# Kernel optimization log

Measured on AMD Instinct MI355X. Metric: run time of the kernel, lower is better.

The kernel has to match this reference:

```python
import jax, jax.numpy as jnp
from jax import lax
import numpy as np

B, T, D_IN, H = 4096, 512, 1, 16


def _lstm_layer(x_seq, W_ih, W_hh, b_ih, b_hh):
    """One LSTM layer, batch_first. x_seq: [B,T,D] -> [B,T,H].
    PyTorch gate order: i, f, g, o. Zero initial (h, c)."""
    H_ = W_hh.shape[1]
    # Precompute input contribution for all timesteps (one big GEMM).
    pre = jnp.einsum('btd,gd->btg', x_seq, W_ih) + b_ih + b_hh  # [B,T,4H]

    def step(carry, p_t):
        h, c = carry
        gates = p_t + h @ W_hh.T  # [B,4H]
        i, f, g, o = jnp.split(gates, 4, axis=-1)
        i = jax.nn.sigmoid(i)
        f = jax.nn.sigmoid(f)
        g = jnp.tanh(g)
        o = jax.nn.sigmoid(o)
        c = f * c + i * g
        h = o * jnp.tanh(c)
        return (h, c), h

    b = x_seq.shape[0]
    init = (jnp.zeros((b, H_), x_seq.dtype), jnp.zeros((b, H_), x_seq.dtype))
    _, hs = lax.scan(step, init, jnp.swapaxes(pre, 0, 1))  # hs: [T,B,H]
    return jnp.swapaxes(hs, 0, 1)


def setup_inputs() -> dict:
    key = jax.random.key(0)
    ks = jax.random.split(key, 11)
    s_ih0 = 1.0 / np.sqrt(H)
    inp = {
        'x': jax.random.normal(ks[0], (B, T, D_IN), dtype=jnp.float32),
        # layer 0: input_dim -> H
        'W_ih0': jax.random.uniform(ks[1], (4 * H, D_IN), jnp.float32, -s_ih0, s_ih0),
        'W_hh0': jax.random.uniform(ks[2], (4 * H, H), jnp.float32, -s_ih0, s_ih0),
        'b_ih0': jax.random.uniform(ks[3], (4 * H,), jnp.float32, -s_ih0, s_ih0),
        'b_hh0': jax.random.uniform(ks[4], (4 * H,), jnp.float32, -s_ih0, s_ih0),
        # layer 1: H -> H
        'W_ih1': jax.random.uniform(ks[5], (4 * H, H), jnp.float32, -s_ih0, s_ih0),
        'W_hh1': jax.random.uniform(ks[6], (4 * H, H), jnp.float32, -s_ih0, s_ih0),
        'b_ih1': jax.random.uniform(ks[7], (4 * H,), jnp.float32, -s_ih0, s_ih0),
        'b_hh1': jax.random.uniform(ks[8], (4 * H,), jnp.float32, -s_ih0, s_ih0),
        # fc head: H -> 1
        'W_fc': jax.random.uniform(ks[9], (1, H), jnp.float32, -s_ih0, s_ih0),
        'b_fc': jax.random.uniform(ks[10], (1,), jnp.float32, -s_ih0, s_ih0),
    }
    return inp


def reference(x, W_ih0, W_hh0, b_ih0, b_hh0, W_ih1, W_hh1, b_ih1, b_hh1, W_fc, b_fc):
    h0 = _lstm_layer(x, W_ih0, W_hh0, b_ih0, b_hh0)   # [B,T,H]
    h1 = _lstm_layer(h0, W_ih1, W_hh1, b_ih1, b_hh1)  # [B,T,H]
    last = h1[:, -1, :]                               # [B,H]
    return last @ W_fc.T + b_fc                       # [B,1]
```

## Files before the change

### kernel.cpp

```cpp
#include <hip/hip_runtime.h>
#include <math.h>

#define TT 512
#define LOG2E 1.4426950408889634f

__device__ __forceinline__ float fast_rcp(float v)  { return __builtin_amdgcn_rcpf(v); }
__device__ __forceinline__ float fast_exp2(float v) { return __builtin_amdgcn_exp2f(v); }

__global__ __launch_bounds__(64, 2)
void lstm2_wave(const float* __restrict__ x,
                const float* __restrict__ W_ih0, const float* __restrict__ W_hh0,
                const float* __restrict__ b_ih0, const float* __restrict__ b_hh0,
                const float* __restrict__ W_ih1, const float* __restrict__ W_hh1,
                const float* __restrict__ b_ih1, const float* __restrict__ b_hh1,
                const float* __restrict__ W_fc,  const float* __restrict__ b_fc,
                float* __restrict__ out)
{
    const int l    = threadIdx.x;
    const int grp  = l >> 5;
    const int half = (l >> 4) & 1;
    const int j    = l & 15;
    const int bid  = blockIdx.x;

    const int ra0 = half * 16 + j;
    const int ra1 = ra0 + 32;

    __shared__ float lds[1168];

    {
        const float4* xg = (const float4*)(x + (size_t)bid * 1024);
        float4* xl = (float4*)&lds[144];
        xl[l]       = xg[l];
        xl[l + 64]  = xg[l + 64];
        xl[l + 128] = xg[l + 128];
        xl[l + 192] = xg[l + 192];
    }
    __syncthreads();

    const float bb0a = b_ih0[ra0] + b_hh0[ra0];
    const float bb0b = b_ih0[ra1] + b_hh0[ra1];
    const float bb1a = b_ih1[ra0] + b_hh1[ra0];
    const float bb1b = b_ih1[ra1] + b_hh1[ra1];
    const float wxa  = W_ih0[ra0];
    const float wxb  = W_ih0[ra1];
    const float Ca1 = half ? (-LOG2E) : (-2.0f * LOG2E);
    const float Aa1 = half ? 1.0f : 2.0f;
    const float Ba1 = half ? 0.0f : -1.0f;
    const float nl2e = -LOG2E;

    const int widx = half ? (80 + grp * 32 + j) : (grp * 40 + j);

    float cs0, cs1 = 0.0f;
    {
        const float x0 = lds[144 + grp * 512];
        const float a_s0 = fmaf(x0, wxa, bb0a);
        const float a_s1 = fmaf(x0, wxb, bb0b);
        const float s0 = fast_rcp(1.0f + fast_exp2(a_s0 * nl2e));
        const float s1 = fmaf(Aa1, fast_rcp(1.0f + fast_exp2(a_s1 * Ca1)), Ba1);
        const float p0 = s0 * s1;
        cs0 = p0;
        const float e = fast_exp2(fabsf(cs0) * (2.0f * LOG2E));
        float th = fmaf(-2.0f, fast_rcp(e + 1.0f), 1.0f);
        th = copysignf(th, cs0);
        const float osw = __shfl_xor(s1, 16);
        const float h0v = osw * th;
        lds[widx]      = h0v;
        lds[widx + 16] = 0.0f;
    }

    {
        unsigned base = (unsigned)(size_t)(void*)&lds[0];
        unsigned hb   = base + grp * 160;
        unsigned xa   = base + 576 + grp * 2048 + 4;
        unsigned wb_  = base + widx * 4;
        const float* pwa = W_hh0 + ra0 * 16;
        const float* pwb = W_ih1 + ra0 * 16;
        const float* pwc = W_hh1 + ra0 * 16;

        asm volatile(
            "s_waitcnt lgkmcnt(0)\n"
            "global_load_dwordx4 v[80:83],   %[pwa], off\n"
            "global_load_dwordx4 v[84:87],   %[pwa], off offset:16\n"
            "global_load_dwordx4 v[88:91],   %[pwa], off offset:32\n"
            "global_load_dwordx4 v[92:95],   %[pwa], off offset:48\n"
            "global_load_dwordx4 v[96:99],   %[pwa], off offset:2048\n"
            "global_load_dwordx4 v[100:103], %[pwa], off offset:2064\n"
            "global_load_dwordx4 v[104:107], %[pwa], off offset:2080\n"
            "global_load_dwordx4 v[108:111], %[pwa], off offset:2096\n"
            "global_load_dwordx4 v[112:115], %[pwb], off\n"
            "global_load_dwordx4 v[116:119], %[pwb], off offset:16\n"
            "global_load_dwordx4 v[120:123], %[pwb], off offset:32\n"
            "global_load_dwordx4 v[124:127], %[pwb], off offset:48\n"
            "global_load_dwordx4 v[128:131], %[pwb], off offset:2048\n"
            "global_load_dwordx4 v[132:135], %[pwb], off offset:2064\n"
            "global_load_dwordx4 v[136:139], %[pwb], off offset:2080\n"
            "global_load_dwordx4 v[140:143], %[pwb], off offset:2096\n"
            "global_load_dwordx4 v[144:147], %[pwc], off\n"
            "global_load_dwordx4 v[148:151], %[pwc], off offset:16\n"
            "global_load_dwordx4 v[152:155], %[pwc], off offset:32\n"
            "global_load_dwordx4 v[156:159], %[pwc], off offset:48\n"
            "global_load_dwordx4 v[160:163], %[pwc], off offset:2048\n"
            "global_load_dwordx4 v[164:167], %[pwc], off offset:2064\n"
            "global_load_dwordx4 v[168:171], %[pwc], off offset:2080\n"
            "global_load_dwordx4 v[172:175], %[pwc], off offset:2096\n"
            "v_mov_b32 v24, %[wb]\n"
            "v_mov_b32 v25, %[hb]\n"
            "v_mov_b32 v26, %[xa]\n"
            "v_mov_b32 v176, %[c0i]\n"
            "v_mov_b32 v177, %[c1]\n"
            "s_movk_i32 s22, 511\n"
            "s_mov_b32 s20, 0x7fffffff\n"
            "s_mov_b32 s21, 0x4038aa3b\n"
            "s_waitcnt vmcnt(0)\n"
            "Llstm_%=:\n"
            "ds_read_b128 v[32:35], v25\n"
            "ds_read_b128 v[36:39], v25 offset:16\n"
            "ds_read_b128 v[40:43], v25 offset:32\n"
            "ds_read_b128 v[44:47], v25 offset:48\n"
            "ds_read_b128 v[48:51], v25 offset:64\n"
            "ds_read_b128 v[52:55], v25 offset:80\n"
            "ds_read_b128 v[56:59], v25 offset:96\n"
            "ds_read_b128 v[60:63], v25 offset:112\n"
            "ds_read_b32  v27, v26\n"
            "v_add_u32 v26, 4, v26\n"
            "s_waitcnt lgkmcnt(5)\n"
            "v_pk_mul_f32 v[64:65], v[80:81],  v[32:33]\n"
            "v_pk_mul_f32 v[66:67], v[96:97],  v[32:33]\n"
            "v_pk_fma_f32 v[64:65], v[82:83],  v[34:35], v[64:65]\n"
            "v_pk_fma_f32 v[66:67], v[98:99],  v[34:35], v[66:67]\n"
            "v_pk_fma_f32 v[64:65], v[84:85],  v[36:37], v[64:65]\n"
            "v_pk_fma_f32 v[66:67], v[100:101], v[36:37], v[66:67]\n"
            "v_pk_fma_f32 v[64:65], v[86:87],  v[38:39], v[64:65]\n"
            "v_pk_fma_f32 v[66:67], v[102:103], v[38:39], v[66:67]\n"
            "v_pk_fma_f32 v[64:65], v[88:89],  v[40:41], v[64:65]\n"
            "v_pk_fma_f32 v[66:67], v[104:105], v[40:41], v[66:67]\n"
            "v_pk_fma_f32 v[64:65], v[90:91],  v[42:43], v[64:65]\n"
            "v_pk_fma_f32 v[66:67], v[106:107], v[42:43], v[66:67]\n"
            "v_pk_fma_f32 v[64:65], v[92:93],  v[44:45], v[64:65]\n"
            "v_pk_fma_f32 v[66:67], v[108:109], v[44:45], v[66:67]\n"
            "v_pk_fma_f32 v[64:65], v[94:95],  v[46:47], v[64:65]\n"
            "v_pk_fma_f32 v[66:67], v[110:111], v[46:47], v[66:67]\n"
            "s_waitcnt lgkmcnt(0)\n"
            "v_add_f32 v28, v64, v65\n"
            "v_add_f32 v29, v66, v67\n"
            "v_add_f32 v28, %[bb0a], v28\n"
            "v_add_f32 v29, %[bb0b], v29\n"
            "v_fmac_f32 v28, v27, %[wxa]\n"
            "v_fmac_f32 v29, v27, %[wxb]\n"
            "v_mul_f32 v72, %[nl2e], v28\n"
            "v_mul_f32 v73, %[Ca1], v29\n"
            "v_exp_f32 v72, v72\n"
            "v_exp_f32 v73, v73\n"
            "v_add_f32 v72, 1.0, v72\n"
            "v_add_f32 v73, 1.0, v73\n"
            "v_rcp_f32 v72, v72\n"
            "v_rcp_f32 v73, v73\n"
            "ds_swizzle_b32 v76, v72 offset:0x401F\n"
            "v_fma_f32 v73, %[Aa1], v73, %[Ba1]\n"
            "ds_swizzle_b32 v77, v73 offset:0x401F\n"
            "v_mul_f32 v28, v72, v73\n"
            "v_pk_mul_f32 v[68:69], v[112:113], v[32:33]\n"
            "v_pk_mul_f32 v[70:71], v[128:129], v[32:33]\n"
            "v_pk_fma_f32 v[68:69], v[114:115], v[34:35], v[68:69]\n"
            "v_pk_fma_f32 v[70:71], v[130:131], v[34:35], v[70:71]\n"
            "v_pk_fma_f32 v[68:69], v[116:117], v[36:37], v[68:69]\n"
            "v_pk_fma_f32 v[70:71], v[132:133], v[36:37], v[70:71]\n"
            "v_pk_fma_f32 v[68:69], v[118:119], v[38:39], v[68:69]\n"
            "v_pk_fma_f32 v[70:71], v[134:135], v[38:39], v[70:71]\n"
            "v_pk_fma_f32 v[68:69], v[120:121], v[40:41], v[68:69]\n"
            "v_pk_fma_f32 v[70:71], v[136:137], v[40:41], v[70:71]\n"
            "v_pk_fma_f32 v[68:69], v[122:123], v[42:43], v[68:69]\n"
            "v_pk_fma_f32 v[70:71], v[138:139], v[42:43], v[70:71]\n"
            "v_pk_fma_f32 v[68:69], v[124:125], v[44:45], v[68:69]\n"
            "v_pk_fma_f32 v[70:71], v[140:141], v[44:45], v[70:71]\n"
            "v_pk_fma_f32 v[68:69], v[126:127], v[46:47], v[68:69]\n"
            "v_pk_fma_f32 v[70:71], v[142:143], v[46:47], v[70:71]\n"
            "v_pk_fma_f32 v[68:69], v[144:145], v[48:49], v[68:69]\n"
            "v_pk_fma_f32 v[70:71], v[160:161], v[48:49], v[70:71]\n"
            "v_pk_fma_f32 v[68:69], v[146:147], v[50:51], v[68:69]\n"
            "v_pk_fma_f32 v[70:71], v[162:163], v[50:51], v[70:71]\n"
            "v_pk_fma_f32 v[68:69], v[148:149], v[52:53], v[68:69]\n"
            "v_pk_fma_f32 v[70:71], v[164:165], v[52:53], v[70:71]\n"
            "v_pk_fma_f32 v[68:69], v[150:151], v[54:55], v[68:69]\n"
            "v_pk_fma_f32 v[70:71], v[166:167], v[54:55], v[70:71]\n"
            "v_pk_fma_f32 v[68:69], v[152:153], v[56:57], v[68:69]\n"
            "v_pk_fma_f32 v[70:71], v[168:169], v[56:57], v[70:71]\n"
            "v_pk_fma_f32 v[68:69], v[154:155], v[58:59], v[68:69]\n"
            "v_pk_fma_f32 v[70:71], v[170:171], v[58:59], v[70:71]\n"
            "v_pk_fma_f32 v[68:69], v[156:157], v[60:61], v[68:69]\n"
            "v_pk_fma_f32 v[70:71], v[172:173], v[60:61], v[70:71]\n"
            "v_pk_fma_f32 v[68:69], v[158:159], v[62:63], v[68:69]\n"
            "v_pk_fma_f32 v[70:71], v[174:175], v[62:63], v[70:71]\n"
            "v_add_f32 v30, v68, v69\n"
            "v_add_f32 v31, v70, v71\n"
            "v_add_f32 v30, %[bb1a], v30\n"
            "v_add_f32 v31, %[bb1b], v31\n"
            "v_mul_f32 v74, %[nl2e], v30\n"
            "v_mul_f32 v75, %[Ca1], v31\n"
            "v_exp_f32 v74, v74\n"
            "v_exp_f32 v75, v75\n"
            "v_add_f32 v74, 1.0, v74\n"
            "v_add_f32 v75, 1.0, v75\n"
            "v_rcp_f32 v74, v74\n"
            "v_rcp_f32 v75, v75\n"
            "ds_swizzle_b32 v78, v74 offset:0x401F\n"
            "v_fma_f32 v75, %[Aa1], v75, %[Ba1]\n"
            "ds_swizzle_b32 v79, v75 offset:0x401F\n"
            "v_mul_f32 v30, v74, v75\n"
            "s_waitcnt lgkmcnt(2)\n"
            "v_fma_f32 v176, v76, v176, v28\n"
            "v_mul_f32 v29, s21, |v176|\n"
            "v_exp_f32 v29, v29\n"
            "s_nop 0\n"
            "v_add_f32 v29, 1.0, v29\n"
            "v_rcp_f32 v29, v29\n"
            "s_nop 0\n"
            "v_fma_f32 v29, -2.0, v29, 1.0\n"
            "v_bfi_b32 v29, s20, v29, v176\n"
            "v_mul_f32 v28, v77, v29\n"
            "ds_write_b32 v24, v28\n"
            "s_waitcnt lgkmcnt(1)\n"
            "v_fma_f32 v177, v78, v177, v30\n"
            "v_mul_f32 v29, s21, |v177|\n"
            "v_exp_f32 v29, v29\n"
            "s_nop 0\n"
            "v_add_f32 v29, 1.0, v29\n"
            "v_rcp_f32 v29, v29\n"
            "s_nop 0\n"
            "v_fma_f32 v29, -2.0, v29, 1.0\n"
            "v_bfi_b32 v29, s20, v29, v177\n"
            "v_mul_f32 v29, v79, v29\n"
            "ds_write_b32 v24, v29 offset:64\n"
            "s_sub_u32 s22, s22, 1\n"
            "s_cmp_lg_u32 s22, 0\n"
            "s_cbranch_scc1 Llstm_%=\n"
            "v_mov_b32 %[c1], v177\n"
            : [c1]"+v"(cs1)
            : [hb]"v"(hb), [xa]"v"(xa), [wb]"v"(wb_),
              [pwa]"v"(pwa), [pwb]"v"(pwb), [pwc]"v"(pwc),
              [bb0a]"v"(bb0a), [bb0b]"v"(bb0b), [bb1a]"v"(bb1a), [bb1b]"v"(bb1b),
              [wxa]"v"(wxa), [wxb]"v"(wxb), [nl2e]"v"(nl2e),
              [Ca1]"v"(Ca1), [Aa1]"v"(Aa1), [Ba1]"v"(Ba1), [c0i]"v"(cs0)
            : "memory", "scc", "s20", "s21", "s22",
              "v24","v25","v26","v27","v28","v29","v30","v31",
              "v32","v33","v34","v35","v36","v37","v38","v39",
              "v40","v41","v42","v43","v44","v45","v46","v47",
              "v48","v49","v50","v51","v52","v53","v54","v55",
              "v56","v57","v58","v59","v60","v61","v62","v63",
              "v64","v65","v66","v67","v68","v69","v70","v71",
              "v72","v73","v74","v75","v76","v77","v78","v79",
              "v80","v81","v82","v83","v84","v85","v86","v87",
              "v88","v89","v90","v91","v92","v93","v94","v95",
              "v96","v97","v98","v99","v100","v101","v102","v103",
              "v104","v105","v106","v107","v108","v109","v110","v111",
              "v112","v113","v114","v115","v116","v117","v118","v119",
              "v120","v121","v122","v123","v124","v125","v126","v127",
              "v128","v129","v130","v131","v132","v133","v134","v135",
              "v136","v137","v138","v139","v140","v141","v142","v143",
              "v144","v145","v146","v147","v148","v149","v150","v151",
              "v152","v153","v154","v155","v156","v157","v158","v159",
              "v160","v161","v162","v163","v164","v165","v166","v167",
              "v168","v169","v170","v171","v172","v173","v174","v175",
              "v176","v177");
    }

    {
        int l2 = __builtin_amdgcn_workitem_id_x();
        asm("" : "+v"(l2));
        const int grp2  = l2 >> 5;
        const int half2 = (l2 >> 4) & 1;
        const int j2    = l2 & 15;
        const int rb0 = half2 * 16 + j2;
        const int rb1 = rb0 + 32;
        const float Ca2 = half2 ? (-LOG2E) : (-2.0f * LOG2E);
        const float Aa2 = half2 ? 1.0f : 2.0f;
        const float Ba2 = half2 ? 0.0f : -1.0f;

        float a1a = b_ih1[rb0] + b_hh1[rb0];
        float a1b = b_ih1[rb1] + b_hh1[rb1];
        const float* h0p = &lds[grp2 * 40];
        const float* h1p = h0p + 16;
        #pragma unroll
        for (int k = 0; k < 16; ++k) {
            const float h0k = h0p[k], h1k = h1p[k];
            a1a = fmaf(W_ih1[rb0 * 16 + k], h0k, a1a);
            a1b = fmaf(W_ih1[rb1 * 16 + k], h0k, a1b);
            a1a = fmaf(W_hh1[rb0 * 16 + k], h1k, a1a);
            a1b = fmaf(W_hh1[rb1 * 16 + k], h1k, a1b);
        }
        const float s0 = fast_rcp(1.0f + fast_exp2(a1a * (-LOG2E)));
        const float s1 = fmaf(Aa2, fast_rcp(1.0f + fast_exp2(a1b * Ca2)), Ba2);
        const float p1  = s0 * s1;
        const float fsw = __shfl_xor(s0, 16);
        const float osw = __shfl_xor(s1, 16);
        const float c1f = fmaf(fsw, cs1, p1);
        const float e = fast_exp2(fabsf(c1f) * (2.0f * LOG2E));
        float th = fmaf(-2.0f, fast_rcp(e + 1.0f), 1.0f);
        th = copysignf(th, c1f);
        const float h1fin = osw * th;

        float p = (half2 == 0) ? h1fin * W_fc[j2] : 0.0f;
        p += __shfl_xor(p, 1);
        p += __shfl_xor(p, 2);
        p += __shfl_xor(p, 4);
        p += __shfl_xor(p, 8);
        p += __shfl_xor(p, 16);
        if ((l2 & 31) == 0) out[2 * bid + grp2] = p + b_fc[0];
    }
}

extern "C" void kernel_launch(void* const* d_in, const int* in_sizes, int n_in,
                              void* d_out, int out_size, void* d_ws, size_t ws_size,
                              hipStream_t stream) {
    const float* x     = (const float*)d_in[0];
    const float* W_ih0 = (const float*)d_in[1];
    const float* W_hh0 = (const float*)d_in[2];
    const float* b_ih0 = (const float*)d_in[3];
    const float* b_hh0 = (const float*)d_in[4];
    const float* W_ih1 = (const float*)d_in[5];
    const float* W_hh1 = (const float*)d_in[6];
    const float* b_ih1 = (const float*)d_in[7];
    const float* b_hh1 = (const float*)d_in[8];
    const float* W_fc  = (const float*)d_in[9];
    const float* b_fc  = (const float*)d_in[10];
    float* out = (float*)d_out;

    dim3 grid(2048), block(64);
    hipLaunchKernelGGL(lstm2_wave, grid, block, 0, stream,
                       x, W_ih0, W_hh0, b_ih0, b_hh0,
                       W_ih1, W_hh1, b_ih1, b_hh1, W_fc, b_fc, out);
}
```

Before: 235.7 us.

## Swap gate-half ownership to need one swizzle per layer and overlap cell update

Reassigns which half-wave owns the cell state so each layer exchanges only the i*g product through one ds_swizzle instead of swizzling both f and o. Biases are folded into the initial packed FMA accumulators, removing the per-step bias adds. LDS waits are split so the FMAs start as each h chunk arrives, and the layer-0 cell/tanh update and h write are interleaved with the layer-1 matvec. The aim is to shorten the serial critical path of each recurrent step, at the cost of eight more VGPRs and a changed lane-to-output mapping that must stay consistent in the final layer.

```diff
diff --git a/kernel.cpp b/kernel.cpp
--- a/kernel.cpp
+++ b/kernel.cpp
@@ -48,7 +48,7 @@
     const float Ba1 = half ? 0.0f : -1.0f;
     const float nl2e = -LOG2E;
 
-    const int widx = half ? (80 + grp * 32 + j) : (grp * 40 + j);
+    const int widx = half ? (grp * 40 + j) : (80 + grp * 32 + j);
 
     float cs0, cs1 = 0.0f;
     {
@@ -57,13 +57,13 @@
         const float a_s1 = fmaf(x0, wxb, bb0b);
         const float s0 = fast_rcp(1.0f + fast_exp2(a_s0 * nl2e));
         const float s1 = fmaf(Aa1, fast_rcp(1.0f + fast_exp2(a_s1 * Ca1)), Ba1);
-        const float p0 = s0 * s1;
-        cs0 = p0;
+        const float p  = s0 * s1;
+        const float psw = __shfl_xor(p, 16);
+        cs0 = psw;
         const float e = fast_exp2(fabsf(cs0) * (2.0f * LOG2E));
         float th = fmaf(-2.0f, fast_rcp(e + 1.0f), 1.0f);
         th = copysignf(th, cs0);
-        const float osw = __shfl_xor(s1, 16);
-        const float h0v = osw * th;
+        const float h0v = s1 * th;
         lds[widx]      = h0v;
         lds[widx + 16] = 0.0f;
     }
@@ -108,11 +108,20 @@
             "v_mov_b32 v26, %[xa]\n"
             "v_mov_b32 v176, %[c0i]\n"
             "v_mov_b32 v177, %[c1]\n"
+            "v_mov_b32 v178, %[bb0a]\n"
+            "v_mov_b32 v179, 0\n"
+            "v_mov_b32 v180, %[bb0b]\n"
+            "v_mov_b32 v181, 0\n"
+            "v_mov_b32 v182, %[bb1a]\n"
+            "v_mov_b32 v183, 0\n"
+            "v_mov_b32 v184, %[bb1b]\n"
+            "v_mov_b32 v185, 0\n"
             "s_movk_i32 s22, 511\n"
             "s_mov_b32 s20, 0x7fffffff\n"
             "s_mov_b32 s21, 0x4038aa3b\n"
             "s_waitcnt vmcnt(0)\n"
             "Llstm_%=:\n"
+            "ds_read_b32  v27, v26\n"
             "ds_read_b128 v[32:35], v25\n"
             "ds_read_b128 v[36:39], v25 offset:16\n"
             "ds_read_b128 v[40:43], v25 offset:32\n"
@@ -121,30 +130,29 @@
             "ds_read_b128 v[52:55], v25 offset:80\n"
             "ds_read_b128 v[56:59], v25 offset:96\n"
             "ds_read_b128 v[60:63], v25 offset:112\n"
-            "ds_read_b32  v27, v26\n"
             "v_add_u32 v26, 4, v26\n"
-            "s_waitcnt lgkmcnt(5)\n"
-            "v_pk_mul_f32 v[64:65], v[80:81],  v[32:33]\n"
-            "v_pk_mul_f32 v[66:67], v[96:97],  v[32:33]\n"
+            "s_waitcnt lgkmcnt(7)\n"
+            "v_pk_fma_f32 v[64:65], v[80:81],  v[32:33], v[178:179]\n"
+            "v_pk_fma_f32 v[66:67], v[96:97],  v[32:33], v[180:181]\n"
             "v_pk_fma_f32 v[64:65], v[82:83],  v[34:35], v[64:65]\n"
             "v_pk_fma_f32 v[66:67], v[98:99],  v[34:35], v[66:67]\n"
+            "s_waitcnt lgkmcnt(6)\n"
             "v_pk_fma_f32 v[64:65], v[84:85],  v[36:37], v[64:65]\n"
             "v_pk_fma_f32 v[66:67], v[100:101], v[36:37], v[66:67]\n"
             "v_pk_fma_f32 v[64:65], v[86:87],  v[38:39], v[64:65]\n"
             "v_pk_fma_f32 v[66:67], v[102:103], v[38:39], v[66:67]\n"
+            "s_waitcnt lgkmcnt(5)\n"
             "v_pk_fma_f32 v[64:65], v[88:89],  v[40:41], v[64:65]\n"
             "v_pk_fma_f32 v[66:67], v[104:105], v[40:41], v[66:67]\n"
             "v_pk_fma_f32 v[64:65], v[90:91],  v[42:43], v[64:65]\n"
             "v_pk_fma_f32 v[66:67], v[106:107], v[42:43], v[66:67]\n"
+            "s_waitcnt lgkmcnt(4)\n"
             "v_pk_fma_f32 v[64:65], v[92:93],  v[44:45], v[64:65]\n"
             "v_pk_fma_f32 v[66:67], v[108:109], v[44:45], v[66:67]\n"
             "v_pk_fma_f32 v[64:65], v[94:95],  v[46:47], v[64:65]\n"
             "v_pk_fma_f32 v[66:67], v[110:111], v[46:47], v[66:67]\n"
-            "s_waitcnt lgkmcnt(0)\n"
             "v_add_f32 v28, v64, v65\n"
             "v_add_f32 v29, v66, v67\n"
-            "v_add_f32 v28, %[bb0a], v28\n"
-            "v_add_f32 v29, %[bb0b], v29\n"
             "v_fmac_f32 v28, v27, %[wxa]\n"
             "v_fmac_f32 v29, v27, %[wxb]\n"
             "v_mul_f32 v72, %[nl2e], v28\n"
@@ -155,12 +163,12 @@
             "v_add_f32 v73, 1.0, v73\n"
             "v_rcp_f32 v72, v72\n"
             "v_rcp_f32 v73, v73\n"
-            "ds_swizzle_b32 v76, v72 offset:0x401F\n"
+            "s_nop 0\n"
             "v_fma_f32 v73, %[Aa1], v73, %[Ba1]\n"
-            "ds_swizzle_b32 v77, v73 offset:0x401F\n"
             "v_mul_f32 v28, v72, v73\n"
-            "v_pk_mul_f32 v[68:69], v[112:113], v[32:33]\n"
-            "v_pk_mul_f32 v[70:71], v[128:129], v[32:33]\n"
+            "ds_swizzle_b32 v76, v28 offset:0x401F\n"
+            "v_pk_fma_f32 v[68:69], v[112:113], v[32:33], v[182:183]\n"
+            "v_pk_fma_f32 v[70:71], v[128:129], v[32:33], v[184:185]\n"
             "v_pk_fma_f32 v[68:69], v[114:115], v[34:35], v[68:69]\n"
             "v_pk_fma_f32 v[70:71], v[130:131], v[34:35], v[70:71]\n"
             "v_pk_fma_f32 v[68:69], v[116:117], v[36:37], v[68:69]\n"
@@ -175,6 +183,18 @@
             "v_pk_fma_f32 v[70:71], v[140:141], v[44:45], v[70:71]\n"
             "v_pk_fma_f32 v[68:69], v[126:127], v[46:47], v[68:69]\n"
             "v_pk_fma_f32 v[70:71], v[142:143], v[46:47], v[70:71]\n"
+            "s_waitcnt lgkmcnt(0)\n"
+            "v_fma_f32 v176, v72, v176, v76\n"
+            "v_mul_f32 v29, s21, |v176|\n"
+            "v_exp_f32 v29, v29\n"
+            "s_nop 0\n"
+            "v_add_f32 v29, 1.0, v29\n"
+            "v_rcp_f32 v29, v29\n"
+            "s_nop 0\n"
+            "v_fma_f32 v29, -2.0, v29, 1.0\n"
+            "v_bfi_b32 v29, s20, v29, v176\n"
+            "v_mul_f32 v28, v73, v29\n"
+            "ds_write_b32 v24, v28\n"
             "v_pk_fma_f32 v[68:69], v[144:145], v[48:49], v[68:69]\n"
             "v_pk_fma_f32 v[70:71], v[160:161], v[48:49], v[70:71]\n"
             "v_pk_fma_f32 v[68:69], v[146:147], v[50:51], v[68:69]\n"
@@ -193,8 +213,6 @@
             "v_pk_fma_f32 v[70:71], v[174:175], v[62:63], v[70:71]\n"
             "v_add_f32 v30, v68, v69\n"
             "v_add_f32 v31, v70, v71\n"
-            "v_add_f32 v30, %[bb1a], v30\n"
-            "v_add_f32 v31, %[bb1b], v31\n"
             "v_mul_f32 v74, %[nl2e], v30\n"
             "v_mul_f32 v75, %[Ca1], v31\n"
             "v_exp_f32 v74, v74\n"
@@ -203,33 +221,21 @@
             "v_add_f32 v75, 1.0, v75\n"
             "v_rcp_f32 v74, v74\n"
             "v_rcp_f32 v75, v75\n"
-            "ds_swizzle_b32 v78, v74 offset:0x401F\n"
+            "s_nop 0\n"
             "v_fma_f32 v75, %[Aa1], v75, %[Ba1]\n"
-            "ds_swizzle_b32 v79, v75 offset:0x401F\n"
             "v_mul_f32 v30, v74, v75\n"
-            "s_waitcnt lgkmcnt(2)\n"
-            "v_fma_f32 v176, v76, v176, v28\n"
-            "v_mul_f32 v29, s21, |v176|\n"
+            "ds_swizzle_b32 v78, v30 offset:0x401F\n"
+            "s_waitcnt lgkmcnt(0)\n"
+            "v_fma_f32 v177, v74, v177, v78\n"
+            "v_mul_f32 v29, s21, |v177|\n"
             "v_exp_f32 v29, v29\n"
             "s_nop 0\n"
             "v_add_f32 v29, 1.0, v29\n"
             "v_rcp_f32 v29, v29\n"
             "s_nop 0\n"
             "v_fma_f32 v29, -2.0, v29, 1.0\n"
-            "v_bfi_b32 v29, s20, v29, v176\n"
-            "v_mul_f32 v28, v77, v29\n"
-            "ds_write_b32 v24, v28\n"
-            "s_waitcnt lgkmcnt(1)\n"
-            "v_fma_f32 v177, v78, v177, v30\n"
-            "v_mul_f32 v29, s21, |v177|\n"
-            "v_exp_f32 v29, v29\n"
-            "s_nop 0\n"
-            "v_add_f32 v29, 1.0, v29\n"
-            "v_rcp_f32 v29, v29\n"
-            "s_nop 0\n"
-            "v_fma_f32 v29, -2.0, v29, 1.0\n"
             "v_bfi_b32 v29, s20, v29, v177\n"
-            "v_mul_f32 v29, v79, v29\n"
+            "v_mul_f32 v29, v75, v29\n"
             "ds_write_b32 v24, v29 offset:64\n"
             "s_sub_u32 s22, s22, 1\n"
             "s_cmp_lg_u32 s22, 0\n"
@@ -261,7 +267,8 @@
               "v152","v153","v154","v155","v156","v157","v158","v159",
               "v160","v161","v162","v163","v164","v165","v166","v167",
               "v168","v169","v170","v171","v172","v173","v174","v175",
-              "v176","v177");
+              "v176","v177","v178","v179","v180","v181","v182","v183",
+              "v184","v185");
     }
 
     {
@@ -291,15 +298,14 @@
         const float s0 = fast_rcp(1.0f + fast_exp2(a1a * (-LOG2E)));
         const float s1 = fmaf(Aa2, fast_rcp(1.0f + fast_exp2(a1b * Ca2)), Ba2);
         const float p1  = s0 * s1;
-        const float fsw = __shfl_xor(s0, 16);
-        const float osw = __shfl_xor(s1, 16);
-        const float c1f = fmaf(fsw, cs1, p1);
+        const float psw = __shfl_xor(p1, 16);
+        const float c1f = fmaf(s0, cs1, psw);
         const float e = fast_exp2(fabsf(c1f) * (2.0f * LOG2E));
         float th = fmaf(-2.0f, fast_rcp(e + 1.0f), 1.0f);
         th = copysignf(th, c1f);
-        const float h1fin = osw * th;
-
-        float p = (half2 == 0) ? h1fin * W_fc[j2] : 0.0f;
+        const float h1fin = s1 * th;
+
+        float p = (half2 == 1) ? h1fin * W_fc[j2] : 0.0f;
         p += __shfl_xor(p, 1);
         p += __shfl_xor(p, 2);
         p += __shfl_xor(p, 4);
```

Result: faster. 229.3 us (-2.7%).
